# Optimization experiments

Hardware: AMD Instinct MI355X
Metric: run time of the kernel (lower is better)

## Reference

```python
import jax, jax.numpy as jnp
import numpy as np

B, S, D_IN = 2, 2048, 1024
HIDDEN, H, HKV = 1024, 16, 4
R = H // HKV          # query heads per kv head
HD = HIDDEN // H      # head_dim = 64
D_OUT = 1024
SCALE = HD ** -0.5


def setup_inputs() -> dict:
    key = jax.random.key(0)
    ks = jax.random.split(key, 5)
    x = jax.random.normal(ks[0], (B, S, D_IN), dtype=jnp.float32)
    # store weights as (in, out); torch Linear computes x @ W.T with W (out,in)
    Wq = jax.random.normal(ks[1], (D_IN, HIDDEN), dtype=jnp.float32) * 0.02
    Wk = jax.random.normal(ks[2], (D_IN, HKV * HD), dtype=jnp.float32) * 0.02
    Wv = jax.random.normal(ks[3], (D_IN, HKV * HD), dtype=jnp.float32) * 0.02
    Wo = jax.random.normal(ks[4], (HIDDEN, D_OUT), dtype=jnp.float32) * 0.02
    return {"x": x, "Wq": Wq, "Wk": Wk, "Wv": Wv, "Wo": Wo}


def reference(x, Wq, Wk, Wv, Wo):
    # projections
    q = x @ Wq                                   # (B,S,H*HD)
    k = x @ Wk                                   # (B,S,HKV*HD)
    v = x @ Wv
    # repeat_interleave maps query head h -> kv head h // R,
    # so split query heads as (HKV, R) groups and broadcast KV.
    q = q.reshape(B, S, HKV, R, HD)
    k = k.reshape(B, S, HKV, HD)
    v = v.reshape(B, S, HKV, HD)
    attn = jnp.einsum('bskrd,btkd->bkrst', q, k) * SCALE   # (B,HKV,R,S,S)
    attn = jax.nn.softmax(attn, axis=-1)
    o = jnp.einsum('bkrst,btkd->bskrd', attn, v)           # (B,S,HKV,R,HD)
    o = o.reshape(B, S, HIDDEN)
    return o @ Wo                                          # (B,S,D_OUT)
```

## Files before the change

kernel.cpp:

```cpp
#include <hip/hip_runtime.h>

using u16 = unsigned short;
using u32 = unsigned int;
typedef __bf16 bf16x8 __attribute__((ext_vector_type(8)));
typedef u16 u16x8 __attribute__((ext_vector_type(8)));
typedef u32 u32x2 __attribute__((ext_vector_type(2)));
typedef u32 u32x4 __attribute__((ext_vector_type(4)));
typedef float f32x4 __attribute__((ext_vector_type(4)));
typedef float f32x16 __attribute__((ext_vector_type(16)));

#define B_   2
#define S_   2048
#define DIN  1024
#define HID  1024
#define NH   16
#define NKV  4
#define HD_  64
#define QKVW 1536
#define QSCL 0.1803368801111244f

__device__ __forceinline__ u16 f2b(float f) {
  u32 u = __builtin_bit_cast(u32, f);
  u32 r = (u + 0x7FFFu + ((u >> 16) & 1u)) >> 16;
  return (u16)r;
}

__device__ __forceinline__ void gl16(const void* g, void* l) {
  __builtin_amdgcn_global_load_lds(
      (const __attribute__((address_space(1))) void*)g,
      (__attribute__((address_space(3))) void*)l, 16, 0, 0);
}

__global__ void k_cvt(const float* __restrict__ in, u16* __restrict__ out, int n8) {
  int i = blockIdx.x * 256 + threadIdx.x;
  if (i >= n8) return;
  const float4* p = (const float4*)(in + (size_t)i * 8);
  float4 a = p[0], b = p[1];
  u16x8 o;
  o[0] = f2b(a.x); o[1] = f2b(a.y); o[2] = f2b(a.z); o[3] = f2b(a.w);
  o[4] = f2b(b.x); o[5] = f2b(b.y); o[6] = f2b(b.z); o[7] = f2b(b.w);
  *(u16x8*)(out + (size_t)i * 8) = o;
}

__global__ __launch_bounds__(256) void k_cvt_t(const float* __restrict__ W, u16* __restrict__ WT, int K, int N) {
  __shared__ float t[32][33];
  const int k0 = blockIdx.x * 32, n0 = blockIdx.y * 32;
  const int c = threadIdx.x & 31, r8 = threadIdx.x >> 5;
#pragma unroll
  for (int i = 0; i < 4; ++i)
    t[r8 + i * 8][c] = W[(size_t)(k0 + r8 + i * 8) * N + n0 + c];
  __syncthreads();
#pragma unroll
  for (int i = 0; i < 4; ++i)
    WT[(size_t)(n0 + r8 + i * 8) * K + k0 + c] = f2b(t[c][r8 + i * 8]);
}

template <typename OutT>
__global__ __launch_bounds__(256) void k_gemm_bt(
    const u16* __restrict__ A, const u16* __restrict__ Bt,
    OutT* __restrict__ C, int M, int N, int K, int scaleCols, float scl)
{
  __shared__ u16 lA[128 * 32];
  __shared__ u16 lB[128 * 32];
  const int tid  = threadIdx.x;
  const int lane = tid & 63;
  const int wave = tid >> 6;
  const int wm = wave >> 1, wn = wave & 1;
  const int g = lane >> 4, li = lane & 15;
  const int bm = blockIdx.y * 128, bn = blockIdx.x * 128;
  const int srow = wave * 16 + (lane >> 2);
  const int scol = (lane & 3) * 8;

  f32x4 acc[4][4];
#pragma unroll
  for (int i = 0; i < 4; ++i)
#pragma unroll
    for (int j = 0; j < 4; ++j) acc[i][j] = f32x4{0.f, 0.f, 0.f, 0.f};

  const u16* Ab = A + (size_t)bm * K;
  const u16* Bb = Bt + (size_t)bn * K;

  for (int k0 = 0; k0 < K; k0 += 32) {
    __syncthreads();
#pragma unroll
    for (int h = 0; h < 2; ++h) {
      gl16(&Ab[(size_t)(h * 64 + srow) * K + k0 + scol], (char*)lA + h * 4096 + wave * 1024);
      gl16(&Bb[(size_t)(h * 64 + srow) * K + k0 + scol], (char*)lB + h * 4096 + wave * 1024);
    }
    __syncthreads();
    bf16x8 af[4], bfr[4];
#pragma unroll
    for (int mt = 0; mt < 4; ++mt)
      af[mt] = *(const bf16x8*)&lA[(wm * 64 + mt * 16 + li) * 32 + g * 8];
#pragma unroll
    for (int nt = 0; nt < 4; ++nt)
      bfr[nt] = *(const bf16x8*)&lB[(wn * 64 + nt * 16 + li) * 32 + g * 8];
    __builtin_amdgcn_s_setprio(1);
#pragma unroll
    for (int mt = 0; mt < 4; ++mt)
#pragma unroll
      for (int nt = 0; nt < 4; ++nt)
        acc[mt][nt] = __builtin_amdgcn_mfma_f32_16x16x32_bf16(af[mt], bfr[nt], acc[mt][nt], 0, 0, 0);
    __builtin_amdgcn_s_setprio(0);
  }

#pragma unroll
  for (int mt = 0; mt < 4; ++mt)
#pragma unroll
    for (int nt = 0; nt < 4; ++nt)
#pragma unroll
      for (int r = 0; r < 4; ++r) {
        int row = bm + wm * 64 + mt * 16 + g * 4 + r;
        int col = bn + wn * 64 + nt * 16 + li;
        float v = acc[mt][nt][r];
        if (col < scaleCols) v *= scl;
        if constexpr (sizeof(OutT) == 4) C[(size_t)row * N + col] = v;
        else                             C[(size_t)row * N + col] = f2b(v);
      }
}

__global__ __launch_bounds__(512, 2) void k_attn(
    const u16* __restrict__ QKV, u16* __restrict__ O)
{
  __shared__ u16 K_lds[2][64 * 64];
  __shared__ u16 Vt_lds[2][64 * 64];
  const int tid  = threadIdx.x;
  const int lane = tid & 63;
  const int w    = tid >> 6;
  const int lq = lane & 31;
  const int hi = lane >> 5;
  const int swl = (lq & 7) << 3;
  const int hx = (hi * 8) ^ (swl & 8);
  const int s0 = blockIdx.x * 64;
  const int kv = blockIdx.y;
  const int b  = blockIdx.z;
  const int hq = kv * 4 + (w & 3);
  const int wq = w >> 2;

  int dcol[4];
#pragma unroll
  for (int d0 = 0; d0 < 4; ++d0) dcol[d0] = (d0 * 16) ^ (swl & 48);

  bf16x8 qf[4];
  {
    const u16* qb = QKV + (size_t)(b * S_ + s0 + wq * 32 + lq) * QKVW + hq * HD_ + hi * 8;
#pragma unroll
    for (int d0 = 0; d0 < 4; ++d0) qf[d0] = *(const bf16x8*)(qb + d0 * 16);
  }

  float l = 0.f;
  f32x16 oacc0 = {}, oacc1 = {};

  const int kt = tid >> 3, kc = (tid & 7) * 8;
  const u16* kgb = QKV + (size_t)(b * S_ + kt) * QKVW + HID + kv * HD_ + kc;
  const int vt = tid & 63, vd = (tid >> 6) * 8;
  const u16* vgb = QKV + (size_t)(b * S_ + vt) * QKVW + HID + NKV * HD_ + kv * HD_ + vd;
  const int kdst = kt * 64 + (kc ^ ((kt & 7) << 3));

  {
    u16x8 kvec = *(const u16x8*)(kgb);
    u16x8 vvec = *(const u16x8*)(vgb);
    *(u16x8*)&K_lds[0][kdst] = kvec;
#pragma unroll
    for (int e = 0; e < 8; ++e)
      Vt_lds[0][(vd + e) * 64 + (vt ^ (((vd + e) & 7) << 3))] = vvec[e];
  }
  __syncthreads();

  constexpr int NT = S_ / 64;
  for (int t = 0; t < NT; ++t) {
    const int cur = t & 1;
    u16x8 kvec, vvec;
    const bool pref = (t + 1 < NT);
    if (pref) {
      kvec = *(const u16x8*)(kgb + (size_t)(t + 1) * 64 * QKVW);
      vvec = *(const u16x8*)(vgb + (size_t)(t + 1) * 64 * QKVW);
    }

    f32x16 st0 = {}, st1 = {};
    __builtin_amdgcn_s_setprio(1);
#pragma unroll
    for (int d0 = 0; d0 < 4; ++d0) {
      bf16x8 kf0 = *(const bf16x8*)&K_lds[cur][lq * 64 + dcol[d0] + hx];
      bf16x8 kf1 = *(const bf16x8*)&K_lds[cur][(32 + lq) * 64 + dcol[d0] + hx];
      st0 = __builtin_amdgcn_mfma_f32_32x32x16_bf16(kf0, qf[d0], st0, 0, 0, 0);
      st1 = __builtin_amdgcn_mfma_f32_32x32x16_bf16(kf1, qf[d0], st1, 0, 0, 0);
    }
    __builtin_amdgcn_s_setprio(0);

#pragma unroll
    for (int i = 0; i < 16; ++i) st0[i] = __builtin_amdgcn_exp2f(st0[i]);
#pragma unroll
    for (int i = 0; i < 16; ++i) st1[i] = __builtin_amdgcn_exp2f(st1[i]);
    float s8[8];
#pragma unroll
    for (int i = 0; i < 8; ++i)
      s8[i] = (st0[i] + st0[i + 8]) + (st1[i] + st1[i + 8]);
    s8[0] += s8[4]; s8[1] += s8[5]; s8[2] += s8[6]; s8[3] += s8[7];
    l += (s8[0] + s8[1]) + (s8[2] + s8[3]);

    bf16x8 pa[4];
#define PK(dst, x, y) asm("v_cvt_pk_bf16_f32 %0, %1, %2" : "=v"(dst) : "v"(x), "v"(y))
#pragma unroll
    for (int kb = 0; kb < 2; ++kb) {
      const f32x16& ev = kb ? st1 : st0;
      u32 a0, a1, b0, b1;
      u32x2 r0, r1;
      u32x4 wv;
      PK(a0, ev[0], ev[1]);  PK(a1, ev[2], ev[3]);
      PK(b0, ev[4], ev[5]);  PK(b1, ev[6], ev[7]);
      r0 = __builtin_amdgcn_permlane32_swap(a0, b0, false, false);
      r1 = __builtin_amdgcn_permlane32_swap(a1, b1, false, false);
      wv[0] = r0[0]; wv[1] = r1[0]; wv[2] = r0[1]; wv[3] = r1[1];
      pa[kb * 2] = __builtin_bit_cast(bf16x8, wv);
      PK(a0, ev[8],  ev[9]);  PK(a1, ev[10], ev[11]);
      PK(b0, ev[12], ev[13]); PK(b1, ev[14], ev[15]);
      r0 = __builtin_amdgcn_permlane32_swap(a0, b0, false, false);
      r1 = __builtin_amdgcn_permlane32_swap(a1, b1, false, false);
      wv[0] = r0[0]; wv[1] = r1[0]; wv[2] = r0[1]; wv[3] = r1[1];
      pa[kb * 2 + 1] = __builtin_bit_cast(bf16x8, wv);
    }
#undef PK

    __builtin_amdgcn_s_setprio(1);
#pragma unroll
    for (int ks = 0; ks < 4; ++ks) {
      bf16x8 vf0 = *(const bf16x8*)&Vt_lds[cur][lq * 64 + dcol[ks] + hx];
      bf16x8 vf1 = *(const bf16x8*)&Vt_lds[cur][(32 + lq) * 64 + dcol[ks] + hx];
      oacc0 = __builtin_amdgcn_mfma_f32_32x32x16_bf16(pa[ks], vf0, oacc0, 0, 0, 0);
      oacc1 = __builtin_amdgcn_mfma_f32_32x32x16_bf16(pa[ks], vf1, oacc1, 0, 0, 0);
    }
    __builtin_amdgcn_s_setprio(0);

    if (pref) {
      *(u16x8*)&K_lds[cur ^ 1][kdst] = kvec;
#pragma unroll
      for (int e = 0; e < 8; ++e)
        Vt_lds[cur ^ 1][(vd + e) * 64 + (vt ^ (((vd + e) & 7) << 3))] = vvec[e];
    }
    __syncthreads();
  }

  l += __shfl_xor(l, 32);
  const size_t obase = (size_t)(b * S_ + s0 + wq * 32) * HID + hq * HD_ + lq;
#pragma unroll
  for (int r = 0; r < 16; ++r) {
    const int qrow = (r & 3) + 8 * (r >> 2) + 4 * hi;
    float lr = __shfl(l, qrow);
    float inv = __builtin_amdgcn_rcpf(lr);
    O[obase + (size_t)qrow * HID]      = f2b(oacc0[r] * inv);
    O[obase + (size_t)qrow * HID + 32] = f2b(oacc1[r] * inv);
  }
}

extern "C" void kernel_launch(void* const* d_in, const int* in_sizes, int n_in,
                              void* d_out, int out_size, void* d_ws, size_t ws_size,
                              hipStream_t stream) {
  (void)in_sizes; (void)n_in; (void)out_size; (void)ws_size;
  const float* x  = (const float*)d_in[0];
  const float* Wq = (const float*)d_in[1];
  const float* Wk = (const float*)d_in[2];
  const float* Wv = (const float*)d_in[3];
  const float* Wo = (const float*)d_in[4];
  float* out = (float*)d_out;

  const size_t M = (size_t)B_ * S_;
  u16* xb    = (u16*)d_ws;
  u16* WqkvT = xb    + M * DIN;
  u16* WoT   = WqkvT + (size_t)QKVW * DIN;
  u16* QKV   = WoT   + (size_t)HID * HID;
  u16* Ob    = QKV   + M * QKVW;

  k_cvt<<<dim3((int)(M * DIN / 8 / 256)), 256, 0, stream>>>(x, xb, (int)(M * DIN / 8));
  k_cvt_t<<<dim3(DIN / 32, HID / 32),       256, 0, stream>>>(Wq, WqkvT,                      DIN, HID);
  k_cvt_t<<<dim3(DIN / 32, (NKV*HD_) / 32), 256, 0, stream>>>(Wk, WqkvT + (size_t)HID * DIN,  DIN, NKV * HD_);
  k_cvt_t<<<dim3(DIN / 32, (NKV*HD_) / 32), 256, 0, stream>>>(Wv, WqkvT + (size_t)(HID + NKV*HD_) * DIN, DIN, NKV * HD_);
  k_cvt_t<<<dim3(HID / 32, HID / 32),       256, 0, stream>>>(Wo, WoT, HID, HID);

  k_gemm_bt<u16><<<dim3(QKVW / 128, (int)(M / 128)), 256, 0, stream>>>(
      xb, WqkvT, QKV, (int)M, QKVW, DIN, HID, QSCL);

  k_attn<<<dim3(S_ / 64, NKV, B_), 512, 0, stream>>>(QKV, Ob);

  k_gemm_bt<float><<<dim3(HID / 128, (int)(M / 128)), 256, 0, stream>>>(
      Ob, WoT, out, (int)M, HID, HID, 0, 1.0f);
}
```

Baseline: 112.7 us.

## Double-buffer GEMM LDS tiles and halve attention block query rows

The GEMM kernel now keeps two LDS stages, so the next K-slice's global-to-LDS load is issued before computing on the current one, leaving one barrier per iteration instead of two. The attention kernel is regrouped into 256-thread blocks covering 32 query rows (4 waves, one per query head in the KV group), with each thread loading twice as much K/V per tile. This doubles the attention grid, which is meant to improve occupancy and load balance across CUs. The cost is that each K/V tile is now fetched by twice as many blocks, and the GEMM uses twice the LDS per block.

```diff
diff --git a/kernel.cpp b/kernel.cpp
--- a/kernel.cpp
+++ b/kernel.cpp
@@ -56,12 +56,12 @@
 }
 
 template <typename OutT>
-__global__ __launch_bounds__(256) void k_gemm_bt(
+__global__ __launch_bounds__(256, 2) void k_gemm_bt(
     const u16* __restrict__ A, const u16* __restrict__ Bt,
     OutT* __restrict__ C, int M, int N, int K, int scaleCols, float scl)
 {
-  __shared__ u16 lA[128 * 32];
-  __shared__ u16 lB[128 * 32];
+  __shared__ u16 lA[2][128 * 32];
+  __shared__ u16 lB[2][128 * 32];
   const int tid  = threadIdx.x;
   const int lane = tid & 63;
   const int wave = tid >> 6;
@@ -80,21 +80,29 @@
   const u16* Ab = A + (size_t)bm * K;
   const u16* Bb = Bt + (size_t)bn * K;
 
+#pragma unroll
+  for (int h = 0; h < 2; ++h) {
+    gl16(&Ab[(size_t)(h * 64 + srow) * K + scol], (char*)lA[0] + h * 4096 + wave * 1024);
+    gl16(&Bb[(size_t)(h * 64 + srow) * K + scol], (char*)lB[0] + h * 4096 + wave * 1024);
+  }
+  __syncthreads();
+
+  int cur = 0;
   for (int k0 = 0; k0 < K; k0 += 32) {
-    __syncthreads();
-#pragma unroll
-    for (int h = 0; h < 2; ++h) {
-      gl16(&Ab[(size_t)(h * 64 + srow) * K + k0 + scol], (char*)lA + h * 4096 + wave * 1024);
-      gl16(&Bb[(size_t)(h * 64 + srow) * K + k0 + scol], (char*)lB + h * 4096 + wave * 1024);
-    }
-    __syncthreads();
+    if (k0 + 32 < K) {
+#pragma unroll
+      for (int h = 0; h < 2; ++h) {
+        gl16(&Ab[(size_t)(h * 64 + srow) * K + k0 + 32 + scol], (char*)lA[cur ^ 1] + h * 4096 + wave * 1024);
+        gl16(&Bb[(size_t)(h * 64 + srow) * K + k0 + 32 + scol], (char*)lB[cur ^ 1] + h * 4096 + wave * 1024);
+      }
+    }
     bf16x8 af[4], bfr[4];
 #pragma unroll
     for (int mt = 0; mt < 4; ++mt)
-      af[mt] = *(const bf16x8*)&lA[(wm * 64 + mt * 16 + li) * 32 + g * 8];
+      af[mt] = *(const bf16x8*)&lA[cur][(wm * 64 + mt * 16 + li) * 32 + g * 8];
 #pragma unroll
     for (int nt = 0; nt < 4; ++nt)
-      bfr[nt] = *(const bf16x8*)&lB[(wn * 64 + nt * 16 + li) * 32 + g * 8];
+      bfr[nt] = *(const bf16x8*)&lB[cur][(wn * 64 + nt * 16 + li) * 32 + g * 8];
     __builtin_amdgcn_s_setprio(1);
 #pragma unroll
     for (int mt = 0; mt < 4; ++mt)
@@ -102,6 +110,8 @@
       for (int nt = 0; nt < 4; ++nt)
         acc[mt][nt] = __builtin_amdgcn_mfma_f32_16x16x32_bf16(af[mt], bfr[nt], acc[mt][nt], 0, 0, 0);
     __builtin_amdgcn_s_setprio(0);
+    __syncthreads();
+    cur ^= 1;
   }
 
 #pragma unroll
@@ -119,7 +129,7 @@
       }
 }
 
-__global__ __launch_bounds__(512, 2) void k_attn(
+__global__ __launch_bounds__(256, 2) void k_attn(
     const u16* __restrict__ QKV, u16* __restrict__ O)
 {
   __shared__ u16 K_lds[2][64 * 64];
@@ -131,11 +141,10 @@
   const int hi = lane >> 5;
   const int swl = (lq & 7) << 3;
   const int hx = (hi * 8) ^ (swl & 8);
-  const int s0 = blockIdx.x * 64;
+  const int s0 = blockIdx.x * 32;
   const int kv = blockIdx.y;
   const int b  = blockIdx.z;
-  const int hq = kv * 4 + (w & 3);
-  const int wq = w >> 2;
+  const int hq = kv * 4 + w;
 
   int dcol[4];
 #pragma unroll
@@ -143,7 +152,7 @@
 
   bf16x8 qf[4];
   {
-    const u16* qb = QKV + (size_t)(b * S_ + s0 + wq * 32 + lq) * QKVW + hq * HD_ + hi * 8;
+    const u16* qb = QKV + (size_t)(b * S_ + s0 + lq) * QKVW + hq * HD_ + hi * 8;
 #pragma unroll
     for (int d0 = 0; d0 < 4; ++d0) qf[d0] = *(const bf16x8*)(qb + d0 * 16);
   }
@@ -158,23 +167,33 @@
   const int kdst = kt * 64 + (kc ^ ((kt & 7) << 3));
 
   {
-    u16x8 kvec = *(const u16x8*)(kgb);
-    u16x8 vvec = *(const u16x8*)(vgb);
-    *(u16x8*)&K_lds[0][kdst] = kvec;
-#pragma unroll
-    for (int e = 0; e < 8; ++e)
-      Vt_lds[0][(vd + e) * 64 + (vt ^ (((vd + e) & 7) << 3))] = vvec[e];
+    u16x8 ka = *(const u16x8*)(kgb);
+    u16x8 kb = *(const u16x8*)(kgb + (size_t)32 * QKVW);
+    u16x8 va = *(const u16x8*)(vgb);
+    u16x8 vb = *(const u16x8*)(vgb + 32);
+    *(u16x8*)&K_lds[0][kdst]           = ka;
+    *(u16x8*)&K_lds[0][kdst + 32 * 64] = kb;
+#pragma unroll
+    for (int e = 0; e < 8; ++e) {
+      const int sz = (vt ^ (((vd + e) & 7) << 3));
+      Vt_lds[0][(vd + e) * 64 + sz]      = va[e];
+      Vt_lds[0][(vd + 32 + e) * 64 + sz] = vb[e];
+    }
   }
   __syncthreads();
 
   constexpr int NT = S_ / 64;
   for (int t = 0; t < NT; ++t) {
     const int cur = t & 1;
-    u16x8 kvec, vvec;
+    u16x8 ka, kb, va, vb;
     const bool pref = (t + 1 < NT);
     if (pref) {
-      kvec = *(const u16x8*)(kgb + (size_t)(t + 1) * 64 * QKVW);
-      vvec = *(const u16x8*)(vgb + (size_t)(t + 1) * 64 * QKVW);
+      const u16* kp = kgb + (size_t)(t + 1) * 64 * QKVW;
+      const u16* vp = vgb + (size_t)(t + 1) * 64 * QKVW;
+      ka = *(const u16x8*)(kp);
+      kb = *(const u16x8*)(kp + (size_t)32 * QKVW);
+      va = *(const u16x8*)(vp);
+      vb = *(const u16x8*)(vp + 32);
     }
 
     f32x16 st0 = {}, st1 = {};
@@ -202,8 +221,8 @@
     bf16x8 pa[4];
 #define PK(dst, x, y) asm("v_cvt_pk_bf16_f32 %0, %1, %2" : "=v"(dst) : "v"(x), "v"(y))
 #pragma unroll
-    for (int kb = 0; kb < 2; ++kb) {
-      const f32x16& ev = kb ? st1 : st0;
+    for (int kb2 = 0; kb2 < 2; ++kb2) {
+      const f32x16& ev = kb2 ? st1 : st0;
       u32 a0, a1, b0, b1;
       u32x2 r0, r1;
       u32x4 wv;
@@ -212,13 +231,13 @@
       r0 = __builtin_amdgcn_permlane32_swap(a0, b0, false, false);
       r1 = __builtin_amdgcn_permlane32_swap(a1, b1, false, false);
       wv[0] = r0[0]; wv[1] = r1[0]; wv[2] = r0[1]; wv[3] = r1[1];
-      pa[kb * 2] = __builtin_bit_cast(bf16x8, wv);
+      pa[kb2 * 2] = __builtin_bit_cast(bf16x8, wv);
       PK(a0, ev[8],  ev[9]);  PK(a1, ev[10], ev[11]);
       PK(b0, ev[12], ev[13]); PK(b1, ev[14], ev[15]);
       r0 = __builtin_amdgcn_permlane32_swap(a0, b0, false, false);
       r1 = __builtin_amdgcn_permlane32_swap(a1, b1, false, false);
       wv[0] = r0[0]; wv[1] = r1[0]; wv[2] = r0[1]; wv[3] = r1[1];
-      pa[kb * 2 + 1] = __builtin_bit_cast(bf16x8, wv);
+      pa[kb2 * 2 + 1] = __builtin_bit_cast(bf16x8, wv);
     }
 #undef PK
 
@@ -233,16 +252,20 @@
     __builtin_amdgcn_s_setprio(0);
 
     if (pref) {
-      *(u16x8*)&K_lds[cur ^ 1][kdst] = kvec;
-#pragma unroll
-      for (int e = 0; e < 8; ++e)
-        Vt_lds[cur ^ 1][(vd + e) * 64 + (vt ^ (((vd + e) & 7) << 3))] = vvec[e];
+      *(u16x8*)&K_lds[cur ^ 1][kdst]           = ka;
+      *(u16x8*)&K_lds[cur ^ 1][kdst + 32 * 64] = kb;
+#pragma unroll
+      for (int e = 0; e < 8; ++e) {
+        const int sz = (vt ^ (((vd + e) & 7) << 3));
+        Vt_lds[cur ^ 1][(vd + e) * 64 + sz]      = va[e];
+        Vt_lds[cur ^ 1][(vd + 32 + e) * 64 + sz] = vb[e];
+      }
     }
     __syncthreads();
   }
 
   l += __shfl_xor(l, 32);
-  const size_t obase = (size_t)(b * S_ + s0 + wq * 32) * HID + hq * HD_ + lq;
+  const size_t obase = (size_t)(b * S_ + s0) * HID + hq * HD_ + lq;
 #pragma unroll
   for (int r = 0; r < 16; ++r) {
     const int qrow = (r & 3) + 8 * (r >> 2) + 4 * hi;
@@ -280,7 +303,7 @@
   k_gemm_bt<u16><<<dim3(QKVW / 128, (int)(M / 128)), 256, 0, stream>>>(
       xb, WqkvT, QKV, (int)M, QKVW, DIN, HID, QSCL);
 
-  k_attn<<<dim3(S_ / 64, NKV, B_), 512, 0, stream>>>(QKV, Ob);
+  k_attn<<<dim3(S_ / 32, NKV, B_), 256, 0, stream>>>(QKV, Ob);
 
   k_gemm_bt<float><<<dim3(HID / 128, (int)(M / 128)), 256, 0, stream>>>(
       Ob, WoT, out, (int)M, HID, HID, 0, 1.0f);
```

Measured after the change: 115.5 us. 1.02x slower.
